# Kernel optimization log

Measured on AMD Instinct MI355X. Metric: run time of the kernel, lower is better.

The kernel has to match this reference:

```python
import jax, jax.numpy as jnp
import numpy as np

N_NODES = 50000
N_EDGES = 1600000
D = 128
LEAKY_SLOPE = 0.01  # torch nn.LeakyReLU default


def setup_inputs() -> dict:
    key = jax.random.key(0)
    ks = jax.random.split(key, 7)
    entity_embed = jax.random.normal(ks[0], (N_NODES, D), dtype=jnp.float32)
    W1 = jax.random.normal(ks[1], (D, D), dtype=jnp.float32) * 0.05
    b1 = jax.random.normal(ks[2], (D,), dtype=jnp.float32) * 0.05
    W2 = jax.random.normal(ks[3], (D, D), dtype=jnp.float32) * 0.05
    b2 = jax.random.normal(ks[4], (D,), dtype=jnp.float32) * 0.05
    src = jax.random.randint(ks[5], (N_EDGES,), 0, N_NODES, dtype=jnp.int32)
    dst = jax.random.randint(ks[6], (N_EDGES,), 0, N_NODES, dtype=jnp.int32)
    return {"entity_embed": entity_embed, "W1": W1, "b1": b1,
            "W2": W2, "b2": b2, "src": src, "dst": dst}


def reference(entity_embed, W1, b1, W2, b2, src, dst):
    # DGL update_all(copy_u('node','side'), sum('side','H')):
    # H[v] = sum over edges (u -> v) of entity_embed[u]
    n = entity_embed.shape[0]
    H = jax.ops.segment_sum(entity_embed[src], dst, num_segments=n)  # [N, D]
    # neighbors branch: LeakyReLU(W_1 @ H)
    neighbors = jax.nn.leaky_relu(H @ W1.T + b1, negative_slope=LEAKY_SLOPE)
    # interactions branch: LeakyReLU(W_2 @ (node * H))
    interactions = jax.nn.leaky_relu((entity_embed * H) @ W2.T + b2,
                                     negative_slope=LEAKY_SLOPE)
    # dropout is identity at inference
    return neighbors + interactions
```

## Files before the change

kernel.cpp:

```cpp
#include <hip/hip_runtime.h>

#define NN 50000
#define DD 128
#define SLOPE 0.01f
#define NB 782
#define BCAP 2560
#define ECH 6144
#define BST 512
#define PB 2
#define OVCAP 8192
#define HP 136

using bf16x8 = __attribute__((ext_vector_type(8))) short;
using f32x4  = __attribute__((ext_vector_type(4))) float;

__device__ inline float bflo(unsigned int w) { return __uint_as_float(w << 16); }
__device__ inline float bfhi(unsigned int w) { return __uint_as_float(w & 0xffff0000u); }
__device__ inline float sbf(short s) {
    return __uint_as_float(((unsigned int)(unsigned short)s) << 16);
}
__device__ inline unsigned int rnebf(float f) {
    unsigned int u = __float_as_uint(f);
    return (u + 0x7fffu + ((u >> 16) & 1u)) >> 16;
}
__device__ inline unsigned int pack2(float lo, float hi) {
    return rnebf(lo) | (rnebf(hi) << 16);
}
__device__ inline uint4 pack8(const float* f) {
    uint4 o;
    o.x = pack2(f[0], f[1]); o.y = pack2(f[2], f[3]);
    o.z = pack2(f[4], f[5]); o.w = pack2(f[6], f[7]);
    return o;
}
__device__ inline void addrow(float* acc, uint4 r) {
    acc[0] += bflo(r.x); acc[1] += bfhi(r.x);
    acc[2] += bflo(r.y); acc[3] += bfhi(r.y);
    acc[4] += bflo(r.z); acc[5] += bfhi(r.z);
    acc[6] += bflo(r.w); acc[7] += bfhi(r.w);
}

__global__ __launch_bounds__(BST) void convert_bin(
    const float* __restrict__ E, const float* __restrict__ W1,
    const float* __restrict__ W2, const int* __restrict__ src,
    const int* __restrict__ dst, unsigned short* __restrict__ Ebf,
    unsigned short* __restrict__ W1b, unsigned short* __restrict__ W2b,
    int* __restrict__ gtail, unsigned int* __restrict__ stag,
    int* __restrict__ ovf_cnt, int2* __restrict__ ovf,
    int n_edges, int nbin)
{
    const int tid = threadIdx.x;

    if (blockIdx.x >= nbin) {
        const int NE8 = NN * DD / 8;
        const int NW8 = DD * DD / 8;
        int t = (blockIdx.x - nbin) * BST + tid;
        const float* s; unsigned short* d; int idx;
        if (t < NE8)                { s = E;  d = Ebf; idx = t; }
        else if (t < NE8 + NW8)     { s = W1; d = W1b; idx = t - NE8; }
        else if (t < NE8 + 2 * NW8) { s = W2; d = W2b; idx = t - NE8 - NW8; }
        else return;
        float4 a = ((const float4*)s)[(size_t)idx * 2];
        float4 b = ((const float4*)s)[(size_t)idx * 2 + 1];
        uint4 o;
        o.x = pack2(a.x, a.y); o.y = pack2(a.z, a.w);
        o.z = pack2(b.x, b.y); o.w = pack2(b.z, b.w);
        ((uint4*)d)[idx] = o;
        return;
    }

    __shared__ unsigned int srt[ECH];
    __shared__ int cnt[NB], off[NB], pos[NB];
    __shared__ int wsum[BST / 64];

    const int e0 = blockIdx.x * ECH;
    const int m = min(ECH, n_edges - e0);

    for (int b = tid; b < NB; b += BST) cnt[b] = 0;
    __syncthreads();

    for (int i = tid; i < m; i += BST)
        atomicAdd(&cnt[dst[e0 + i] >> 6], 1);
    __syncthreads();

    const int lane = tid & 63, w = tid >> 6;
    int b0 = tid * PB;
    int loc[PB]; int s = 0;
    #pragma unroll
    for (int j = 0; j < PB; ++j) {
        int bb = b0 + j;
        int cv = (bb < NB) ? cnt[bb] : 0;
        loc[j] = s; s += cv;
    }
    int incl = s;
    #pragma unroll
    for (int d = 1; d < 64; d <<= 1) {
        int t2 = __shfl_up(incl, d);
        if (lane >= d) incl += t2;
    }
    if (lane == 63) wsum[w] = incl;
    __syncthreads();
    int wbase = 0;
    for (int w2 = 0; w2 < w; ++w2) wbase += wsum[w2];
    int base = wbase + incl - s;
    #pragma unroll
    for (int j = 0; j < PB; ++j) {
        int bb = b0 + j;
        if (bb < NB) { off[bb] = base + loc[j]; pos[bb] = base + loc[j]; }
    }
    __syncthreads();

    for (int i = tid; i < m; i += BST) {
        int v = dst[e0 + i];
        int u = src[e0 + i];
        int p = atomicAdd(&pos[v >> 6], 1);
        srt[p] = (unsigned int)u | ((unsigned int)(v & 63) << 16);
    }
    __syncthreads();

    for (int bb = tid; bb < NB; bb += BST) {
        int c = cnt[bb];
        if (!c) continue;
        int g = atomicAdd(&gtail[bb], c);
        int s0 = off[bb];
        unsigned int* dstp = stag + (size_t)bb * BCAP;
        for (int k = 0; k < c; ++k) {
            int gp = g + k;
            unsigned int r = srt[s0 + k];
            if (gp < BCAP) {
                dstp[gp] = r;
            } else {
                int oi = atomicAdd(ovf_cnt, 1);
                if (oi < OVCAP)
                    ovf[oi] = make_int2((int)(r & 0xffffu),
                                        bb * 64 + (int)((r >> 16) & 63));
            }
        }
    }
}

__global__ __launch_bounds__(256) void bucket_fused(
    const unsigned short* __restrict__ Ebf, const int* __restrict__ gtail,
    const unsigned int* __restrict__ stag, const int* __restrict__ ovf_cnt,
    const int2* __restrict__ ovf,
    const unsigned short* __restrict__ W1b, const unsigned short* __restrict__ W2b,
    const float* __restrict__ b1, const float* __restrict__ b2,
    float* __restrict__ out)
{
    __shared__ unsigned short sorted[BCAP];
    __shared__ unsigned short Hs[64][HP];
    __shared__ int cnt[64], off[65], pos[64];
    __shared__ int s_novf;

    const int b = blockIdx.x;
    const int tid = threadIdx.x;
    int len = gtail[b]; len = len < BCAP ? len : BCAP;
    const unsigned int* seg = stag + (size_t)b * BCAP;

    if (tid == 0) { int t = *ovf_cnt; s_novf = t < OVCAP ? t : OVCAP; }
    if (tid < 64) cnt[tid] = 0;
    __syncthreads();
    for (int i = tid; i < len; i += 256)
        atomicAdd(&cnt[(seg[i] >> 16) & 63], 1);
    __syncthreads();
    if (tid == 0) {
        int a = 0;
        for (int j = 0; j < 64; ++j) { off[j] = a; pos[j] = a; a += cnt[j]; }
        off[64] = a;
    }
    __syncthreads();
    for (int i = tid; i < len; i += 256) {
        unsigned int r = seg[i];
        int p = atomicAdd(&pos[(r >> 16) & 63], 1);
        sorted[p] = (unsigned short)(r & 0xffffu);
    }
    __syncthreads();
    const int novf = s_novf;

    const int g = tid >> 4;
    const int c = tid & 15;
    const uint4* E4 = (const uint4*)Ebf;
    for (int p4 = 0; p4 < 4; ++p4) {
        int nl = p4 * 16 + g;
        int v = b * 64 + nl;
        if (v >= NN) continue;
        float acc[8] = {};
        int i = off[nl], e1 = off[nl + 1];
        for (; i + 8 <= e1; i += 8) {
            uint4 r0 = E4[(size_t)sorted[i]     * 16 + c];
            uint4 r1 = E4[(size_t)sorted[i + 1] * 16 + c];
            uint4 r2 = E4[(size_t)sorted[i + 2] * 16 + c];
            uint4 r3 = E4[(size_t)sorted[i + 3] * 16 + c];
            uint4 r4 = E4[(size_t)sorted[i + 4] * 16 + c];
            uint4 r5 = E4[(size_t)sorted[i + 5] * 16 + c];
            uint4 r6 = E4[(size_t)sorted[i + 6] * 16 + c];
            uint4 r7 = E4[(size_t)sorted[i + 7] * 16 + c];
            addrow(acc, r0); addrow(acc, r1); addrow(acc, r2); addrow(acc, r3);
            addrow(acc, r4); addrow(acc, r5); addrow(acc, r6); addrow(acc, r7);
        }
        for (; i + 2 <= e1; i += 2) {
            uint4 r0 = E4[(size_t)sorted[i]     * 16 + c];
            uint4 r1 = E4[(size_t)sorted[i + 1] * 16 + c];
            addrow(acc, r0); addrow(acc, r1);
        }
        if (i < e1) addrow(acc, E4[(size_t)sorted[i] * 16 + c]);

        if (novf > 0) {
            for (int k = 0; k < novf; ++k) {
                int2 e = ovf[k];
                if (e.y == v) addrow(acc, E4[(size_t)e.x * 16 + c]);
            }
        }
        *(uint4*)&Hs[nl][c * 8] = pack8(acc);
    }
    __syncthreads();

    const int wave = tid >> 6;
    const int lane = tid & 63;
    const int v0 = b * 64 + wave * 16;
    if (v0 >= NN) return;
    const int m = lane & 15;
    const int quad = lane >> 4;

    bf16x8 aH[4], aE[4];
    const unsigned short* hrow = &Hs[wave * 16 + m][quad * 8];
    const unsigned short* erow = Ebf + (size_t)(v0 + m) * DD + quad * 8;
    #pragma unroll
    for (int ks = 0; ks < 4; ++ks) {
        bf16x8 h8 = *(const bf16x8*)(hrow + ks * 32);
        bf16x8 e8 = *(const bf16x8*)(erow + ks * 32);
        aH[ks] = h8;
        bf16x8 eh;
        #pragma unroll
        for (int j = 0; j < 8; ++j)
            eh[j] = (short)rnebf(sbf(h8[j]) * sbf(e8[j]));
        aE[ks] = eh;
    }

    #pragma unroll
    for (int jt = 0; jt < 8; ++jt) {
        const int j0 = jt * 16;
        const unsigned short* w1r = W1b + (size_t)(j0 + m) * DD + quad * 8;
        const unsigned short* w2r = W2b + (size_t)(j0 + m) * DD + quad * 8;
        f32x4 acc1 = {0.f, 0.f, 0.f, 0.f}, acc2 = {0.f, 0.f, 0.f, 0.f};
        #pragma unroll
        for (int ks = 0; ks < 4; ++ks) {
            bf16x8 bw1 = *(const bf16x8*)(w1r + ks * 32);
            bf16x8 bw2 = *(const bf16x8*)(w2r + ks * 32);
            acc1 = __builtin_amdgcn_mfma_f32_16x16x32_bf16(aH[ks], bw1, acc1, 0, 0, 0);
            acc2 = __builtin_amdgcn_mfma_f32_16x16x32_bf16(aE[ks], bw2, acc2, 0, 0, 0);
        }
        const float bb1 = b1[j0 + m], bb2 = b2[j0 + m];
        #pragma unroll
        for (int i = 0; i < 4; ++i) {
            int row = v0 + quad * 4 + i;
            if (row < NN) {
                float x1 = acc1[i] + bb1; x1 = x1 > 0.f ? x1 : SLOPE * x1;
                float x2 = acc2[i] + bb2; x2 = x2 > 0.f ? x2 : SLOPE * x2;
                out[(size_t)row * DD + j0 + m] = x1 + x2;
            }
        }
    }
}

__global__ __launch_bounds__(256) void scatter_add(
    const float* __restrict__ E, const int* __restrict__ src,
    const int* __restrict__ dst, float* __restrict__ H, int n_edges)
{
    int t = blockIdx.x * 256 + threadIdx.x;
    int e = t >> 5;
    if (e >= n_edges) return;
    int c = t & 31;
    float4 a = ((const float4*)E)[(size_t)src[e] * 32 + c];
    float* hp = H + (size_t)dst[e] * DD + c * 4;
    atomicAdd(hp + 0, a.x); atomicAdd(hp + 1, a.y);
    atomicAdd(hp + 2, a.z); atomicAdd(hp + 3, a.w);
}

__global__ __launch_bounds__(256) void fused_mlp(
    const float* __restrict__ E, const float* __restrict__ H,
    const float* __restrict__ W1, const float* __restrict__ b1,
    const float* __restrict__ W2, const float* __restrict__ b2,
    float* __restrict__ out)
{
    __shared__ float Hsf[32][DD];
    __shared__ float EHs[32][DD];
    __shared__ float W1s[DD][20];
    __shared__ float W2s[DD][20];
    const int tid = threadIdx.x;
    const int v0 = blockIdx.x * 32;
    const int nvalid = min(32, NN - v0);
    for (int i = 0; i < 4; ++i) {
        int f = tid + 256 * i;
        int n = f >> 5, c = f & 31;
        float4 h = make_float4(0.f, 0.f, 0.f, 0.f);
        float4 eh = h;
        if (n < nvalid) {
            h = ((const float4*)H)[(size_t)(v0 + n) * 32 + c];
            float4 e4 = ((const float4*)E)[(size_t)(v0 + n) * 32 + c];
            eh = make_float4(e4.x * h.x, e4.y * h.y, e4.z * h.z, e4.w * h.w);
        }
        *((float4*)&Hsf[n][c * 4]) = h;
        *((float4*)&EHs[n][c * 4]) = eh;
    }
    const int jg = tid & 63;
    const int n0 = (tid >> 6) * 8;
    float acc1a[8] = {}, acc1b[8] = {}, acc2a[8] = {}, acc2b[8] = {};
    for (int t8 = 0; t8 < 8; ++t8) {
        const int k0 = t8 * 16;
        __syncthreads();
        for (int i = 0; i < 8; ++i) {
            int f = tid + 256 * i;
            int j = f >> 4, kk = f & 15;
            W1s[j][kk] = W1[j * DD + k0 + kk];
            W2s[j][kk] = W2[j * DD + k0 + kk];
        }
        __syncthreads();
        for (int c = 0; c < 4; ++c) {
            float4 w1a = *((const float4*)&W1s[jg][c * 4]);
            float4 w1b = *((const float4*)&W1s[jg + 64][c * 4]);
            float4 w2a = *((const float4*)&W2s[jg][c * 4]);
            float4 w2b = *((const float4*)&W2s[jg + 64][c * 4]);
            const int kk = k0 + c * 4;
            for (int n = 0; n < 8; ++n) {
                float4 h = *((const float4*)&Hsf[n0 + n][kk]);
                float4 eh = *((const float4*)&EHs[n0 + n][kk]);
                acc1a[n] += h.x * w1a.x + h.y * w1a.y + h.z * w1a.z + h.w * w1a.w;
                acc1b[n] += h.x * w1b.x + h.y * w1b.y + h.z * w1b.z + h.w * w1b.w;
                acc2a[n] += eh.x * w2a.x + eh.y * w2a.y + eh.z * w2a.z + eh.w * w2a.w;
                acc2b[n] += eh.x * w2b.x + eh.y * w2b.y + eh.z * w2b.z + eh.w * w2b.w;
            }
        }
    }
    const float b1a = b1[jg], b1b = b1[jg + 64];
    const float b2a = b2[jg], b2b = b2[jg + 64];
    for (int n = 0; n < 8; ++n) {
        if (n0 + n < nvalid) {
            const int v = v0 + n0 + n;
            float x1 = acc1a[n] + b1a; x1 = x1 > 0.f ? x1 : SLOPE * x1;
            float x2 = acc2a[n] + b2a; x2 = x2 > 0.f ? x2 : SLOPE * x2;
            out[(size_t)v * DD + jg] = x1 + x2;
            float y1 = acc1b[n] + b1b; y1 = y1 > 0.f ? y1 : SLOPE * y1;
            float y2 = acc2b[n] + b2b; y2 = y2 > 0.f ? y2 : SLOPE * y2;
            out[(size_t)v * DD + jg + 64] = y1 + y2;
        }
    }
}

extern "C" void kernel_launch(void* const* d_in, const int* in_sizes, int n_in,
                              void* d_out, int out_size, void* d_ws, size_t ws_size,
                              hipStream_t stream)
{
    const float* E  = (const float*)d_in[0];
    const float* W1 = (const float*)d_in[1];
    const float* b1 = (const float*)d_in[2];
    const float* W2 = (const float*)d_in[3];
    const float* b2 = (const float*)d_in[4];
    const int* src  = (const int*)d_in[5];
    const int* dst  = (const int*)d_in[6];
    float* out = (float*)d_out;
    const int n_edges = in_sizes[5];

    char* ws = (char*)d_ws;
    auto al = [](size_t x) { return (x + 255) & ~(size_t)255; };

    const size_t off_tail = 0;
    const size_t off_ovfc = (size_t)NB * 4;
    const size_t off_ovf  = al(off_ovfc + 4);
    const size_t off_stag = al(off_ovf + (size_t)OVCAP * 8);
    const size_t off_Ebf  = al(off_stag + (size_t)NB * BCAP * 4);
    const size_t off_W1b  = al(off_Ebf + (size_t)NN * DD * 2);
    const size_t off_W2b  = al(off_W1b + (size_t)DD * DD * 2);
    const size_t need_bf  = off_W2b + (size_t)DD * DD * 2;

    if (ws_size >= need_bf) {
        int*  gtail   = (int*)(ws + off_tail);
        int*  ovf_cnt = (int*)(ws + off_ovfc);
        int2* ovf     = (int2*)(ws + off_ovf);
        unsigned int*   stag = (unsigned int*)(ws + off_stag);
        unsigned short* Ebf  = (unsigned short*)(ws + off_Ebf);
        unsigned short* W1b  = (unsigned short*)(ws + off_W1b);
        unsigned short* W2b  = (unsigned short*)(ws + off_W2b);

        const int nbin = (n_edges + ECH - 1) / ECH;
        const int ncv  = NN * DD / 8 + 2 * (DD * DD / 8);
        const int ncvb = (ncv + BST - 1) / BST;

        hipMemsetAsync(ws, 0, off_ovf, stream);
        convert_bin<<<nbin + ncvb, BST, 0, stream>>>(
            E, W1, W2, src, dst, Ebf, W1b, W2b,
            gtail, stag, ovf_cnt, ovf, n_edges, nbin);
        bucket_fused<<<NB, 256, 0, stream>>>(
            Ebf, gtail, stag, ovf_cnt, ovf, W1b, W2b, b1, b2, out);
        return;
    }

    const size_t hbytes = (size_t)NN * DD * sizeof(float);
    float* H = (ws_size >= hbytes) ? (float*)ws : out;
    hipMemsetAsync(H, 0, hbytes, stream);
    scatter_add<<<((n_edges * 32) + 255) / 256, 256, 0, stream>>>(
        E, src, dst, H, n_edges);
    fused_mlp<<<(NN + 31) / 32, 256, 0, stream>>>(E, H, W1, b1, W2, b2, out);
}
```

Before: 197.4 us.

## Fuse memset, binning, conversion and bucket MLP into one cooperative kernel

Adds a persistent cooperative kernel with one block per bucket. It zeroes the counters, bins edges (2048 per block, held in registers), converts E/W1/W2 to bf16 with a grid-stride loop, then runs the per-bucket gather plus MFMA MLP after a grid-wide sync. Shared memory for the two phases is overlaid with a union. This removes the memset and the separate kernel launches, along with the gaps between them. In exchange it adds two grid syncs, runs conversion with fewer threads, and increases global atomic traffic on the bucket tails because the binning chunks are smaller. The old multi-kernel path stays as a fallback if the cooperative launch fails.

```diff
diff --git a/kernel.cpp b/kernel.cpp
--- a/kernel.cpp
+++ b/kernel.cpp
@@ -1,15 +1,20 @@
 #include <hip/hip_runtime.h>
+#include <hip/hip_cooperative_groups.h>
+
+namespace cg = cooperative_groups;
 
 #define NN 50000
 #define DD 128
 #define SLOPE 0.01f
 #define NB 782
 #define BCAP 2560
-#define ECH 6144
-#define BST 512
-#define PB 2
+#define ECH 2048
+#define EPT 8
 #define OVCAP 8192
 #define HP 136
+#define FECH 6144
+#define BST 512
+#define PB2 2
 
 using bf16x8 = __attribute__((ext_vector_type(8))) short;
 using f32x4  = __attribute__((ext_vector_type(4))) float;
@@ -26,7 +31,7 @@
 __device__ inline unsigned int pack2(float lo, float hi) {
     return rnebf(lo) | (rnebf(hi) << 16);
 }
-__device__ inline uint4 pack8(const float* f) {
+__device__ inline uint4 pack8f(const float* f) {
     uint4 o;
     o.x = pack2(f[0], f[1]); o.y = pack2(f[2], f[3]);
     o.z = pack2(f[4], f[5]); o.w = pack2(f[6], f[7]);
@@ -37,6 +42,251 @@
     acc[2] += bflo(r.y); acc[3] += bfhi(r.y);
     acc[4] += bflo(r.z); acc[5] += bfhi(r.z);
     acc[6] += bflo(r.w); acc[7] += bfhi(r.w);
+}
+
+struct P1 {
+    unsigned int srt[ECH];
+    int off[NB];
+    int pos[NB];
+    int wsum[4];
+};
+struct P2 {
+    unsigned short sorted[BCAP];
+    unsigned short Hs[64][HP];
+    int cnt[64]; int off2[65]; int pos2[64];
+};
+
+__global__ __launch_bounds__(256, 4) void mega(
+    const float* __restrict__ E, const float* __restrict__ W1,
+    const float* __restrict__ W2,
+    const float* __restrict__ b1, const float* __restrict__ b2,
+    const int* __restrict__ src, const int* __restrict__ dst, int n_edges,
+    unsigned short* __restrict__ Ebf, unsigned short* __restrict__ W1b,
+    unsigned short* __restrict__ W2b,
+    int* __restrict__ gtail, unsigned int* __restrict__ stag,
+    int* __restrict__ ovf_cnt, int2* __restrict__ ovf,
+    float* __restrict__ out)
+{
+    __shared__ union ShU { P1 p1; P2 p2; } sh;
+    __shared__ int s_novf;
+
+    cg::grid_group grid = cg::this_grid();
+    const int tid = threadIdx.x;
+    const int bid = blockIdx.x;
+    const int gid = bid * 256 + tid;
+    const int gsz = gridDim.x * 256;
+
+    for (int i = gid; i < NB; i += gsz) gtail[i] = 0;
+    if (gid == 0) *ovf_cnt = 0;
+    grid.sync();
+
+    {
+        const int e0 = bid * ECH;
+        const int m = min(ECH, n_edges - e0);
+        int uu[EPT], vv[EPT];
+        #pragma unroll
+        for (int k = 0; k < EPT; ++k) {
+            int i = tid + 256 * k;
+            if (i < m) { uu[k] = src[e0 + i]; vv[k] = dst[e0 + i]; }
+            else vv[k] = -1;
+        }
+        for (int b = tid; b < NB; b += 256) sh.p1.pos[b] = 0;
+        __syncthreads();
+        #pragma unroll
+        for (int k = 0; k < EPT; ++k)
+            if (vv[k] >= 0) atomicAdd(&sh.p1.pos[vv[k] >> 6], 1);
+        __syncthreads();
+
+        const int lane = tid & 63, w = tid >> 6;
+        int b0 = tid * 4;
+        int loc[4]; int s = 0;
+        #pragma unroll
+        for (int j = 0; j < 4; ++j) {
+            int bb = b0 + j;
+            int cv = (bb < NB) ? sh.p1.pos[bb] : 0;
+            loc[j] = s; s += cv;
+        }
+        int incl = s;
+        #pragma unroll
+        for (int d = 1; d < 64; d <<= 1) {
+            int t2 = __shfl_up(incl, d);
+            if (lane >= d) incl += t2;
+        }
+        if (lane == 63) sh.p1.wsum[w] = incl;
+        __syncthreads();
+        int wbase = 0;
+        for (int w2 = 0; w2 < w; ++w2) wbase += sh.p1.wsum[w2];
+        int base = wbase + incl - s;
+        #pragma unroll
+        for (int j = 0; j < 4; ++j) {
+            int bb = b0 + j;
+            if (bb < NB) { sh.p1.off[bb] = base + loc[j]; sh.p1.pos[bb] = base + loc[j]; }
+        }
+        __syncthreads();
+
+        #pragma unroll
+        for (int k = 0; k < EPT; ++k) {
+            if (vv[k] >= 0) {
+                int p = atomicAdd(&sh.p1.pos[vv[k] >> 6], 1);
+                sh.p1.srt[p] = (unsigned int)uu[k]
+                             | ((unsigned int)(vv[k] & 63) << 16);
+            }
+        }
+        __syncthreads();
+
+        for (int bb = tid; bb < NB; bb += 256) {
+            int s0 = sh.p1.off[bb], e1 = sh.p1.pos[bb];
+            int c = e1 - s0;
+            if (!c) continue;
+            int g = atomicAdd(&gtail[bb], c);
+            unsigned int* dstp = stag + (size_t)bb * BCAP;
+            for (int k = 0; k < c; ++k) {
+                int gp = g + k;
+                unsigned int r = sh.p1.srt[s0 + k];
+                if (gp < BCAP) {
+                    dstp[gp] = r;
+                } else {
+                    int oi = atomicAdd(ovf_cnt, 1);
+                    if (oi < OVCAP)
+                        ovf[oi] = make_int2((int)(r & 0xffffu),
+                                            bb * 64 + (int)((r >> 16) & 63));
+                }
+            }
+        }
+    }
+
+    {
+        const int NE8 = NN * DD / 8;
+        const int NW8 = DD * DD / 8;
+        const int NCV = NE8 + 2 * NW8;
+        for (int t = gid; t < NCV; t += gsz) {
+            const float* s2; unsigned short* d2; int idx;
+            if (t < NE8)            { s2 = E;  d2 = Ebf; idx = t; }
+            else if (t < NE8 + NW8) { s2 = W1; d2 = W1b; idx = t - NE8; }
+            else                    { s2 = W2; d2 = W2b; idx = t - NE8 - NW8; }
+            float4 a = ((const float4*)s2)[(size_t)idx * 2];
+            float4 b = ((const float4*)s2)[(size_t)idx * 2 + 1];
+            uint4 o;
+            o.x = pack2(a.x, a.y); o.y = pack2(a.z, a.w);
+            o.z = pack2(b.x, b.y); o.w = pack2(b.z, b.w);
+            ((uint4*)d2)[idx] = o;
+        }
+    }
+
+    grid.sync();
+
+    const int b = bid;
+    int len = gtail[b]; len = len < BCAP ? len : BCAP;
+    const unsigned int* seg = stag + (size_t)b * BCAP;
+
+    if (tid == 0) { int t = *ovf_cnt; s_novf = t < OVCAP ? t : OVCAP; }
+    if (tid < 64) sh.p2.cnt[tid] = 0;
+    __syncthreads();
+    for (int i = tid; i < len; i += 256)
+        atomicAdd(&sh.p2.cnt[(seg[i] >> 16) & 63], 1);
+    __syncthreads();
+    if (tid == 0) {
+        int a = 0;
+        for (int j = 0; j < 64; ++j) {
+            sh.p2.off2[j] = a; sh.p2.pos2[j] = a; a += sh.p2.cnt[j];
+        }
+        sh.p2.off2[64] = a;
+    }
+    __syncthreads();
+    for (int i = tid; i < len; i += 256) {
+        unsigned int r = seg[i];
+        int p = atomicAdd(&sh.p2.pos2[(r >> 16) & 63], 1);
+        sh.p2.sorted[p] = (unsigned short)(r & 0xffffu);
+    }
+    __syncthreads();
+    const int novf = s_novf;
+
+    {
+        const int g = tid >> 4;
+        const int c = tid & 15;
+        const uint4* E4 = (const uint4*)Ebf;
+        for (int p4 = 0; p4 < 4; ++p4) {
+            int nl = p4 * 16 + g;
+            int v = b * 64 + nl;
+            if (v >= NN) continue;
+            float acc[8] = {};
+            int i = sh.p2.off2[nl], e1 = sh.p2.off2[nl + 1];
+            for (; i + 8 <= e1; i += 8) {
+                uint4 r0 = E4[(size_t)sh.p2.sorted[i]     * 16 + c];
+                uint4 r1 = E4[(size_t)sh.p2.sorted[i + 1] * 16 + c];
+                uint4 r2 = E4[(size_t)sh.p2.sorted[i + 2] * 16 + c];
+                uint4 r3 = E4[(size_t)sh.p2.sorted[i + 3] * 16 + c];
+                uint4 r4 = E4[(size_t)sh.p2.sorted[i + 4] * 16 + c];
+                uint4 r5 = E4[(size_t)sh.p2.sorted[i + 5] * 16 + c];
+                uint4 r6 = E4[(size_t)sh.p2.sorted[i + 6] * 16 + c];
+                uint4 r7 = E4[(size_t)sh.p2.sorted[i + 7] * 16 + c];
+                addrow(acc, r0); addrow(acc, r1); addrow(acc, r2); addrow(acc, r3);
+                addrow(acc, r4); addrow(acc, r5); addrow(acc, r6); addrow(acc, r7);
+            }
+            for (; i + 2 <= e1; i += 2) {
+                uint4 r0 = E4[(size_t)sh.p2.sorted[i]     * 16 + c];
+                uint4 r1 = E4[(size_t)sh.p2.sorted[i + 1] * 16 + c];
+                addrow(acc, r0); addrow(acc, r1);
+            }
+            if (i < e1) addrow(acc, E4[(size_t)sh.p2.sorted[i] * 16 + c]);
+
+            if (novf > 0) {
+                for (int k = 0; k < novf; ++k) {
+                    int2 e = ovf[k];
+                    if (e.y == v) addrow(acc, E4[(size_t)e.x * 16 + c]);
+                }
+            }
+            *(uint4*)&sh.p2.Hs[nl][c * 8] = pack8f(acc);
+        }
+    }
+    __syncthreads();
+
+    const int wave = tid >> 6;
+    const int lane = tid & 63;
+    const int v0 = b * 64 + wave * 16;
+    if (v0 >= NN) return;
+    const int m = lane & 15;
+    const int quad = lane >> 4;
+
+    bf16x8 aH[4], aE[4];
+    const unsigned short* hrow = &sh.p2.Hs[wave * 16 + m][quad * 8];
+    const unsigned short* erow = Ebf + (size_t)(v0 + m) * DD + quad * 8;
+    #pragma unroll
+    for (int ks = 0; ks < 4; ++ks) {
+        bf16x8 h8 = *(const bf16x8*)(hrow + ks * 32);
+        bf16x8 e8 = *(const bf16x8*)(erow + ks * 32);
+        aH[ks] = h8;
+        bf16x8 eh;
+        #pragma unroll
+        for (int j = 0; j < 8; ++j)
+            eh[j] = (short)rnebf(sbf(h8[j]) * sbf(e8[j]));
+        aE[ks] = eh;
+    }
+
+    #pragma unroll
+    for (int jt = 0; jt < 8; ++jt) {
+        const int j0 = jt * 16;
+        const unsigned short* w1r = W1b + (size_t)(j0 + m) * DD + quad * 8;
+        const unsigned short* w2r = W2b + (size_t)(j0 + m) * DD + quad * 8;
+        f32x4 acc1 = {0.f, 0.f, 0.f, 0.f}, acc2 = {0.f, 0.f, 0.f, 0.f};
+        #pragma unroll
+        for (int ks = 0; ks < 4; ++ks) {
+            bf16x8 bw1 = *(const bf16x8*)(w1r + ks * 32);
+            bf16x8 bw2 = *(const bf16x8*)(w2r + ks * 32);
+            acc1 = __builtin_amdgcn_mfma_f32_16x16x32_bf16(aH[ks], bw1, acc1, 0, 0, 0);
+            acc2 = __builtin_amdgcn_mfma_f32_16x16x32_bf16(aE[ks], bw2, acc2, 0, 0, 0);
+        }
+        const float bb1 = b1[j0 + m], bb2 = b2[j0 + m];
+        #pragma unroll
+        for (int i = 0; i < 4; ++i) {
+            int row = v0 + quad * 4 + i;
+            if (row < NN) {
+                float x1 = acc1[i] + bb1; x1 = x1 > 0.f ? x1 : SLOPE * x1;
+                float x2 = acc2[i] + bb2; x2 = x2 > 0.f ? x2 : SLOPE * x2;
+                out[(size_t)row * DD + j0 + m] = x1 + x2;
+            }
+        }
+    }
 }
 
 __global__ __launch_bounds__(BST) void convert_bin(
@@ -49,7 +299,6 @@
     int n_edges, int nbin)
 {
     const int tid = threadIdx.x;
-
     if (blockIdx.x >= nbin) {
         const int NE8 = NN * DD / 8;
         const int NW8 = DD * DD / 8;
@@ -67,26 +316,21 @@
         ((uint4*)d)[idx] = o;
         return;
     }
-
-    __shared__ unsigned int srt[ECH];
+    __shared__ unsigned int srt[FECH];
     __shared__ int cnt[NB], off[NB], pos[NB];
     __shared__ int wsum[BST / 64];
-
-    const int e0 = blockIdx.x * ECH;
-    const int m = min(ECH, n_edges - e0);
-
+    const int e0 = blockIdx.x * FECH;
+    const int m = min(FECH, n_edges - e0);
     for (int b = tid; b < NB; b += BST) cnt[b] = 0;
     __syncthreads();
-
     for (int i = tid; i < m; i += BST)
         atomicAdd(&cnt[dst[e0 + i] >> 6], 1);
     __syncthreads();
-
     const int lane = tid & 63, w = tid >> 6;
-    int b0 = tid * PB;
-    int loc[PB]; int s = 0;
+    int b0 = tid * PB2;
+    int loc[PB2]; int s = 0;
     #pragma unroll
-    for (int j = 0; j < PB; ++j) {
+    for (int j = 0; j < PB2; ++j) {
         int bb = b0 + j;
         int cv = (bb < NB) ? cnt[bb] : 0;
         loc[j] = s; s += cv;
@@ -103,12 +347,11 @@
     for (int w2 = 0; w2 < w; ++w2) wbase += wsum[w2];
     int base = wbase + incl - s;
     #pragma unroll
-    for (int j = 0; j < PB; ++j) {
+    for (int j = 0; j < PB2; ++j) {
         int bb = b0 + j;
         if (bb < NB) { off[bb] = base + loc[j]; pos[bb] = base + loc[j]; }
     }
     __syncthreads();
-
     for (int i = tid; i < m; i += BST) {
         int v = dst[e0 + i];
         int u = src[e0 + i];
@@ -116,7 +359,6 @@
         srt[p] = (unsigned int)u | ((unsigned int)(v & 63) << 16);
     }
     __syncthreads();
-
     for (int bb = tid; bb < NB; bb += BST) {
         int c = cnt[bb];
         if (!c) continue;
@@ -126,9 +368,8 @@
         for (int k = 0; k < c; ++k) {
             int gp = g + k;
             unsigned int r = srt[s0 + k];
-            if (gp < BCAP) {
-                dstp[gp] = r;
-            } else {
+            if (gp < BCAP) dstp[gp] = r;
+            else {
                 int oi = atomicAdd(ovf_cnt, 1);
                 if (oi < OVCAP)
                     ovf[oi] = make_int2((int)(r & 0xffffu),
@@ -150,12 +391,10 @@
     __shared__ unsigned short Hs[64][HP];
     __shared__ int cnt[64], off[65], pos[64];
     __shared__ int s_novf;
-
     const int b = blockIdx.x;
     const int tid = threadIdx.x;
     int len = gtail[b]; len = len < BCAP ? len : BCAP;
     const unsigned int* seg = stag + (size_t)b * BCAP;
-
     if (tid == 0) { int t = *ovf_cnt; s_novf = t < OVCAP ? t : OVCAP; }
     if (tid < 64) cnt[tid] = 0;
     __syncthreads();
@@ -175,7 +414,6 @@
     }
     __syncthreads();
     const int novf = s_novf;
-
     const int g = tid >> 4;
     const int c = tid & 15;
     const uint4* E4 = (const uint4*)Ebf;
@@ -203,24 +441,21 @@
             addrow(acc, r0); addrow(acc, r1);
         }
         if (i < e1) addrow(acc, E4[(size_t)sorted[i] * 16 + c]);
-
         if (novf > 0) {
             for (int k = 0; k < novf; ++k) {
                 int2 e = ovf[k];
                 if (e.y == v) addrow(acc, E4[(size_t)e.x * 16 + c]);
             }
         }
-        *(uint4*)&Hs[nl][c * 8] = pack8(acc);
-    }
-    __syncthreads();
-
+        *(uint4*)&Hs[nl][c * 8] = pack8f(acc);
+    }
+    __syncthreads();
     const int wave = tid >> 6;
     const int lane = tid & 63;
     const int v0 = b * 64 + wave * 16;
     if (v0 >= NN) return;
     const int m = lane & 15;
     const int quad = lane >> 4;
-
     bf16x8 aH[4], aE[4];
     const unsigned short* hrow = &Hs[wave * 16 + m][quad * 8];
     const unsigned short* erow = Ebf + (size_t)(v0 + m) * DD + quad * 8;
@@ -235,7 +470,6 @@
             eh[j] = (short)rnebf(sbf(h8[j]) * sbf(e8[j]));
         aE[ks] = eh;
     }
-
     #pragma unroll
     for (int jt = 0; jt < 8; ++jt) {
         const int j0 = jt * 16;
@@ -358,7 +592,7 @@
     const int* src  = (const int*)d_in[5];
     const int* dst  = (const int*)d_in[6];
     float* out = (float*)d_out;
-    const int n_edges = in_sizes[5];
+    int n_edges = in_sizes[5];
 
     char* ws = (char*)d_ws;
     auto al = [](size_t x) { return (x + 255) & ~(size_t)255; };
@@ -381,10 +615,25 @@
         unsigned short* W1b  = (unsigned short*)(ws + off_W1b);
         unsigned short* W2b  = (unsigned short*)(ws + off_W2b);
 
-        const int nbin = (n_edges + ECH - 1) / ECH;
+        int dev = 0, coop = 0;
+        hipGetDevice(&dev);
+        hipDeviceGetAttribute(&coop, hipDeviceAttributeCooperativeLaunch, dev);
+        if (coop) {
+            void* args[] = {
+                (void*)&E, (void*)&W1, (void*)&W2, (void*)&b1, (void*)&b2,
+                (void*)&src, (void*)&dst, (void*)&n_edges,
+                (void*)&Ebf, (void*)&W1b, (void*)&W2b,
+                (void*)&gtail, (void*)&stag, (void*)&ovf_cnt, (void*)&ovf,
+                (void*)&out
+            };
+            hipError_t err = hipLaunchCooperativeKernel(
+                (const void*)mega, dim3(NB), dim3(256), args, 0, stream);
+            if (err == hipSuccess) return;
+        }
+
+        const int nbin = (n_edges + FECH - 1) / FECH;
         const int ncv  = NN * DD / 8 + 2 * (DD * DD / 8);
         const int ncvb = (ncv + BST - 1) / BST;
-
         hipMemsetAsync(ws, 0, off_ovf, stream);
         convert_bin<<<nbin + ncvb, BST, 0, stream>>>(
             E, W1, W2, src, dst, Ebf, W1b, W2b,
```

Result: slower. 359.6 us (+82.2%).
